# Kernel tuning notes

Measured on AMD Instinct MI355X. Metric: run time of the kernel, lower is better.

## Reference

```python
import jax, jax.numpy as jnp
import numpy as np

B, T, S, C, E, H = 4, 2048, 2048, 256, 512, 8
D = E // H
SCALE = E ** (-0.5)


def setup_inputs() -> dict:
    key = jax.random.key(0)
    ks = jax.random.split(key, 12)
    x = jax.random.normal(ks[0], (B, T, C), dtype=jnp.float32)
    context = jax.random.normal(ks[1], (B, S, E), dtype=jnp.float32)
    pad_mask = jax.random.randint(ks[2], (B, T, S), 0, 2) == 1
    p = 0.02
    # Conv1d kernel_size=1 weights stored squeezed: [out_ch, in_ch]
    w_in = jax.random.normal(ks[3], (E, C), dtype=jnp.float32) * p
    b_in = jnp.zeros((E,), dtype=jnp.float32)
    wq = jax.random.normal(ks[4], (E, E), dtype=jnp.float32) * p
    bq = jnp.zeros((E,), dtype=jnp.float32)
    wk = jax.random.normal(ks[5], (E, E), dtype=jnp.float32) * p
    bk = jnp.zeros((E,), dtype=jnp.float32)
    wv = jax.random.normal(ks[6], (E, E), dtype=jnp.float32) * p
    bv = jnp.zeros((E,), dtype=jnp.float32)
    w_out = jax.random.normal(ks[7], (C, E), dtype=jnp.float32) * p
    b_out = jnp.zeros((C,), dtype=jnp.float32)
    return {"x": x, "context": context, "pad_mask": pad_mask,
            "w_in": w_in, "b_in": b_in, "wq": wq, "bq": bq,
            "wk": wk, "bk": bk, "wv": wv, "bv": bv,
            "w_out": w_out, "b_out": b_out}


def reference(x, context, pad_mask, w_in, b_in, wq, bq, wk, bk, wv, bv, w_out, b_out):
    # proj_in: Conv1d k=1 == per-token linear on channel dim. [B,T,C] -> [B,T,E]
    xe = jnp.einsum('btc,ec->bte', x, w_in) + b_in
    Q = (xe @ wq.T + bq).reshape(B, T, H, D)       # query tokens
    K = (context @ wk.T + bk).reshape(B, S, H, D)  # key tokens
    V = (context @ wv.T + bv).reshape(B, S, H, D)
    att = jnp.einsum('bihd,bjhd->bhij', Q, K) * SCALE  # [B,H,T,S]
    att = jnp.where(pad_mask[:, None, :, :], jnp.float32(-1e9), att)
    att = jax.nn.softmax(att, axis=-1)
    out = jnp.einsum('bhij,bjhd->bihd', att, V).reshape(B, T, E)
    # proj_out: Conv1d k=1, [B,T,E] -> [B,T,C]
    out = jnp.einsum('bte,ce->btc', out, w_out) + b_out
    return out
```

## Files before the change

### kernel.cpp

```cpp
#include <hip/hip_runtime.h>
#include <cstdint>
#include <cstddef>

#define Bb 4
#define Tt 2048
#define Ssz 2048
#define Cc 256
#define Ee 512
#define Hh 8

typedef short bf8 __attribute__((ext_vector_type(8)));
typedef float f4 __attribute__((ext_vector_type(4)));

__device__ __forceinline__ unsigned short f2bf(float x) {
  unsigned int u = __float_as_uint(x);
  u += 0x7fffu + ((u >> 16) & 1u);
  return (unsigned short)(u >> 16);
}

__device__ __forceinline__ bf8 cvt8(float4 a, float4 b) {
  bf8 r;
  r[0] = (short)f2bf(a.x); r[1] = (short)f2bf(a.y);
  r[2] = (short)f2bf(a.z); r[3] = (short)f2bf(a.w);
  r[4] = (short)f2bf(b.x); r[5] = (short)f2bf(b.y);
  r[6] = (short)f2bf(b.z); r[7] = (short)f2bf(b.w);
  return r;
}

__global__ __launch_bounds__(256) void prep(const float* __restrict__ w_in,
                                            const float* __restrict__ b_in,
                                            const float* __restrict__ wq,
                                            const float* __restrict__ bq,
                                            const float* __restrict__ wk,
                                            const float* __restrict__ wv,
                                            const float* __restrict__ wo,
                                            unsigned short* __restrict__ wkvb,
                                            unsigned short* __restrict__ wob,
                                            unsigned short* __restrict__ wqin,
                                            float* __restrict__ bqinb, float qsc) {
  __shared__ unsigned short sh[128][72];
  const int bid = blockIdx.x, tid = threadIdx.x;
  if (bid < 512) {
    int i = bid * 256 + tid;
    const float* s = (i < 65536) ? wk : wv;
    int off = (i < 65536) ? i : i - 65536;
    float4 v = ((const float4*)s)[off];
    ushort4 o;
    o.x = f2bf(v.x); o.y = f2bf(v.y); o.z = f2bf(v.z); o.w = f2bf(v.w);
    ((ushort4*)wkvb)[i] = o;
  } else if (bid < 640) {
    int i = (bid - 512) * 256 + tid;
    float4 v = ((const float4*)wo)[i];
    ushort4 o;
    o.x = f2bf(v.x); o.y = f2bf(v.y); o.z = f2bf(v.z); o.w = f2bf(v.w);
    ((ushort4*)wob)[i] = o;
  } else if (bid < 672) {
    const int idx = bid - 640;
    const int m0 = (idx & 7) * 64, n0 = (idx >> 3) * 64;
    unsigned short (*As)[72] = (unsigned short (*)[72]) & sh[0][0];
    unsigned short (*Bs)[72] = (unsigned short (*)[72]) & sh[64][0];
    const int wave = tid >> 6, lane = tid & 63;
    const int lrow = lane & 15, quad = lane >> 4;
    const int wm = (wave >> 1) * 32, wn = (wave & 1) * 32;
    const int arow = tid >> 3, ac = tid & 7;
    f4 acc[2][2];
#pragma unroll
    for (int i = 0; i < 2; i++)
#pragma unroll
      for (int j = 0; j < 2; j++) {
        f4 z = {0.f, 0.f, 0.f, 0.f};
        acc[i][j] = z;
      }
    for (int kt = 0; kt < 8; kt++) {
#pragma unroll
      for (int i = 0; i < 2; i++) {
        int row = arow + i * 32;
        const float* src = wq + (size_t)(m0 + row) * Ee + kt * 64 + ac * 8;
        float4 v0 = *(const float4*)src, v1 = *(const float4*)(src + 4);
        bf8 av;
        av[0] = (short)f2bf(v0.x * qsc); av[1] = (short)f2bf(v0.y * qsc);
        av[2] = (short)f2bf(v0.z * qsc); av[3] = (short)f2bf(v0.w * qsc);
        av[4] = (short)f2bf(v1.x * qsc); av[5] = (short)f2bf(v1.y * qsc);
        av[6] = (short)f2bf(v1.z * qsc); av[7] = (short)f2bf(v1.w * qsc);
        *(bf8*)&As[row][ac * 8] = av;
        int c = n0 + row;
        bf8 bv;
#pragma unroll
        for (int k = 0; k < 8; k++)
          bv[k] = (short)f2bf(w_in[(size_t)(kt * 64 + ac * 8 + k) * Cc + c]);
        *(bf8*)&Bs[row][ac * 8] = bv;
      }
      __syncthreads();
#pragma unroll
      for (int kk = 0; kk < 2; kk++) {
        bf8 af[2], bff[2];
#pragma unroll
        for (int i = 0; i < 2; i++) af[i] = *(const bf8*)&As[wm + i * 16 + lrow][kk * 32 + quad * 8];
#pragma unroll
        for (int j = 0; j < 2; j++) bff[j] = *(const bf8*)&Bs[wn + j * 16 + lrow][kk * 32 + quad * 8];
#pragma unroll
        for (int i = 0; i < 2; i++)
#pragma unroll
          for (int j = 0; j < 2; j++)
            acc[i][j] = __builtin_amdgcn_mfma_f32_16x16x32_bf16(af[i], bff[j], acc[i][j], 0, 0, 0);
      }
      __syncthreads();
    }
#pragma unroll
    for (int j = 0; j < 2; j++)
#pragma unroll
      for (int i = 0; i < 2; i++)
#pragma unroll
        for (int r = 0; r < 4; r++)
          wqin[(size_t)(m0 + wm + i * 16 + quad * 4 + r) * Cc + n0 + wn + j * 16 + lrow] =
              f2bf(acc[i][j][r]);
  } else {
    const int o = (bid - 672) * 32 + (tid >> 3);
    const int k0 = (tid & 7) * 64;
    float s = 0.f;
#pragma unroll
    for (int i = 0; i < 16; i++) {
      float4 w = *(const float4*)(wq + (size_t)o * Ee + k0 + i * 4);
      float4 bb = *(const float4*)(b_in + k0 + i * 4);
      s += w.x * bb.x + w.y * bb.y + w.z * bb.z + w.w * bb.w;
    }
    s += __shfl_xor(s, 1);
    s += __shfl_xor(s, 2);
    s += __shfl_xor(s, 4);
    if ((tid & 7) == 0) bqinb[o] = (s + bq[o]) * qsc;
  }
}

__global__ __launch_bounds__(256) void qkv(const float* __restrict__ x,
                                           const float* __restrict__ ctx,
                                           const unsigned short* __restrict__ wqin,
                                           const float* __restrict__ bqinb,
                                           const unsigned short* __restrict__ wkv,
                                           const float* __restrict__ bk,
                                           const float* __restrict__ bv,
                                           unsigned short* __restrict__ Qb,
                                           unsigned short* __restrict__ Kb,
                                           unsigned short* __restrict__ Vt,
                                           const int* __restrict__ mask,
                                           unsigned int* __restrict__ mp) {
  __shared__ unsigned short As[128][72];
  __shared__ unsigned short Bs[128][72];
  const int bid = blockIdx.x, tid = threadIdx.x;
  if (bid >= 768) {
    int i = (bid - 768) * 256 + tid;
    const int4* src = (const int4*)mask + (size_t)i * 8;
    unsigned int w = 0;
#pragma unroll
    for (int k = 0; k < 8; k++) {
      int4 v = src[k];
      w |= (unsigned int)(v.x != 0) << (k * 4);
      w |= (unsigned int)(v.y != 0) << (k * 4 + 1);
      w |= (unsigned int)(v.z != 0) << (k * 4 + 2);
      w |= (unsigned int)(v.w != 0) << (k * 4 + 3);
    }
    mp[i] = w;
    return;
  }
  const bool isQ = bid < 256;
  const int idx = isQ ? bid : bid - 256;
  const int m0 = (idx & 63) * 128;
  const int n0 = (idx >> 6) * 128;
  const int K = isQ ? 256 : 512;
  const float* A = isQ ? x : ctx;
  const unsigned short* Bt = isQ ? wqin : wkv;

  const int wave = tid >> 6, lane = tid & 63;
  const int lrow = lane & 15, quad = lane >> 4;
  const int wm = (wave >> 1) * 64, wn = (wave & 1) * 64;
  const int arow = tid >> 3, ac = tid & 7;

  f4 acc[4][4];
#pragma unroll
  for (int i = 0; i < 4; i++)
#pragma unroll
    for (int j = 0; j < 4; j++) {
      f4 z = {0.f, 0.f, 0.f, 0.f};
      acc[i][j] = z;
    }

  float4 ap0[4], ap1[4];
  bf8 bpre[4];
#pragma unroll
  for (int i = 0; i < 4; i++) {
    const float* src = A + (size_t)(m0 + arow + i * 32) * K + ac * 8;
    ap0[i] = *(const float4*)src;
    ap1[i] = *(const float4*)(src + 4);
    bpre[i] = *(const bf8*)(Bt + (size_t)(n0 + arow + i * 32) * K + ac * 8);
  }

  const int nkt = K >> 6;
  for (int kt = 0; kt < nkt; ++kt) {
#pragma unroll
    for (int i = 0; i < 4; i++) {
      *(bf8*)&As[arow + i * 32][ac * 8] = cvt8(ap0[i], ap1[i]);
      *(bf8*)&Bs[arow + i * 32][ac * 8] = bpre[i];
    }
    __syncthreads();
    if (kt + 1 < nkt) {
      int k0 = (kt + 1) << 6;
#pragma unroll
      for (int i = 0; i < 4; i++) {
        const float* src = A + (size_t)(m0 + arow + i * 32) * K + k0 + ac * 8;
        ap0[i] = *(const float4*)src;
        ap1[i] = *(const float4*)(src + 4);
        bpre[i] = *(const bf8*)(Bt + (size_t)(n0 + arow + i * 32) * K + k0 + ac * 8);
      }
    }
#pragma unroll
    for (int kk = 0; kk < 2; kk++) {
      bf8 af[4], bff[4];
#pragma unroll
      for (int i = 0; i < 4; i++)
        af[i] = *(const bf8*)&As[wm + i * 16 + lrow][kk * 32 + quad * 8];
#pragma unroll
      for (int j = 0; j < 4; j++)
        bff[j] = *(const bf8*)&Bs[wn + j * 16 + lrow][kk * 32 + quad * 8];
#pragma unroll
      for (int i = 0; i < 4; i++)
#pragma unroll
        for (int j = 0; j < 4; j++)
          acc[i][j] = __builtin_amdgcn_mfma_f32_16x16x32_bf16(af[i], bff[j],
                                                              acc[i][j], 0, 0, 0);
    }
    __syncthreads();
  }

  if (isQ) {
#pragma unroll
    for (int j = 0; j < 4; j++) {
      int col = n0 + wn + j * 16 + lrow;
      float bvv = bqinb[col];
#pragma unroll
      for (int i = 0; i < 4; i++)
#pragma unroll
        for (int r = 0; r < 4; r++)
          Qb[(size_t)(m0 + wm + i * 16 + quad * 4 + r) * Ee + col] =
              f2bf(acc[i][j][r] + bvv);
    }
  } else if (n0 < 512) {
#pragma unroll
    for (int j = 0; j < 4; j++) {
      int col = n0 + wn + j * 16 + lrow;
      float bvv = bk[col];
#pragma unroll
      for (int i = 0; i < 4; i++)
#pragma unroll
        for (int r = 0; r < 4; r++)
          Kb[(size_t)(m0 + wm + i * 16 + quad * 4 + r) * Ee + col] =
              f2bf(acc[i][j][r] + bvv);
    }
  } else {
#pragma unroll
    for (int j = 0; j < 4; j++) {
      int d = n0 - 512 + wn + j * 16 + lrow;
      int h = d >> 6, dd = d & 63;
      float bvv = bv[d];
#pragma unroll
      for (int i = 0; i < 4; i++) {
        int tok = m0 + wm + i * 16 + quad * 4;
        int b = tok >> 11, sl = tok & 2047;
        ushort4 pk;
        pk.x = f2bf(acc[i][j][0] + bvv);
        pk.y = f2bf(acc[i][j][1] + bvv);
        pk.z = f2bf(acc[i][j][2] + bvv);
        pk.w = f2bf(acc[i][j][3] + bvv);
        *(ushort4*)(Vt + (size_t)((b * Hh + h) * 64 + dd) * Ssz + sl) = pk;
      }
    }
  }
}

template <bool OUT_BF16, int BM, int BN, int WGM>
__global__ __launch_bounds__(256) void gemm_bt(const unsigned short* __restrict__ A,
                                               const unsigned short* __restrict__ Bt,
                                               const float* __restrict__ bias0,
                                               void* __restrict__ Cout,
                                               int M, int N, int K) {
  constexpr int WGN = 4 / WGM;
  constexpr int MI = BM / (WGM * 16);
  constexpr int NJ = BN / (WGN * 16);
  constexpr int NA = BM / 32;
  constexpr int NB = BN / 32;
  __shared__ unsigned short As[BM][72];
  __shared__ unsigned short Bs[BN][72];
  const int tid = threadIdx.x;
  const int wave = tid >> 6, lane = tid & 63;
  const int lrow = lane & 15, quad = lane >> 4;
  const int wm = (wave / WGN) * (BM / WGM);
  const int wn = (wave % WGN) * (BN / WGN);
  const int m0 = blockIdx.x * BM, n0 = blockIdx.y * BN;
  const int arow = tid >> 3, ac = tid & 7;

  f4 acc[MI][NJ];
#pragma unroll
  for (int i = 0; i < MI; i++)
#pragma unroll
    for (int j = 0; j < NJ; j++) {
      f4 z = {0.f, 0.f, 0.f, 0.f};
      acc[i][j] = z;
    }

  bf8 apre[NA], bpre[NB];
#pragma unroll
  for (int i = 0; i < NA; i++)
    apre[i] = *(const bf8*)(A + (size_t)(m0 + arow + i * 32) * K + ac * 8);
#pragma unroll
  for (int i = 0; i < NB; i++)
    bpre[i] = *(const bf8*)(Bt + (size_t)(n0 + arow + i * 32) * K + ac * 8);

  const int nkt = K >> 6;
  for (int kt = 0; kt < nkt; ++kt) {
#pragma unroll
    for (int i = 0; i < NA; i++) *(bf8*)&As[arow + i * 32][ac * 8] = apre[i];
#pragma unroll
    for (int i = 0; i < NB; i++) *(bf8*)&Bs[arow + i * 32][ac * 8] = bpre[i];
    __syncthreads();
    if (kt + 1 < nkt) {
      int k0 = (kt + 1) << 6;
#pragma unroll
      for (int i = 0; i < NA; i++)
        apre[i] = *(const bf8*)(A + (size_t)(m0 + arow + i * 32) * K + k0 + ac * 8);
#pragma unroll
      for (int i = 0; i < NB; i++)
        bpre[i] = *(const bf8*)(Bt + (size_t)(n0 + arow + i * 32) * K + k0 + ac * 8);
    }
#pragma unroll
    for (int kk = 0; kk < 2; kk++) {
      bf8 af[MI], bff[NJ];
#pragma unroll
      for (int i = 0; i < MI; i++)
        af[i] = *(const bf8*)&As[wm + i * 16 + lrow][kk * 32 + quad * 8];
#pragma unroll
      for (int j = 0; j < NJ; j++)
        bff[j] = *(const bf8*)&Bs[wn + j * 16 + lrow][kk * 32 + quad * 8];
#pragma unroll
      for (int i = 0; i < MI; i++)
#pragma unroll
        for (int j = 0; j < NJ; j++)
          acc[i][j] = __builtin_amdgcn_mfma_f32_16x16x32_bf16(af[i], bff[j],
                                                              acc[i][j], 0, 0, 0);
    }
    __syncthreads();
  }

#pragma unroll
  for (int j = 0; j < NJ; j++) {
    int col = n0 + wn + j * 16 + lrow;
    float bvv = bias0 ? bias0[col] : 0.f;
#pragma unroll
    for (int i = 0; i < MI; i++) {
#pragma unroll
      for (int r = 0; r < 4; r++) {
        int row = m0 + wm + i * 16 + quad * 4 + r;
        float v = acc[i][j][r] + bvv;
        if (OUT_BF16)
          ((unsigned short*)Cout)[(size_t)row * N + col] = f2bf(v);
        else
          ((float*)Cout)[(size_t)row * N + col] = v;
      }
    }
  }
}

__global__ __launch_bounds__(256) void attn(const unsigned short* __restrict__ Q,
                                            const unsigned short* __restrict__ K,
                                            const unsigned short* __restrict__ Vt,
                                            const unsigned int* __restrict__ mp,
                                            unsigned short* __restrict__ O) {
  __shared__ unsigned short Ks[64][72];
  __shared__ unsigned short Vts[64][72];
  __shared__ unsigned short Ps[128][72];
  const int tid = threadIdx.x;
  const int wave = tid >> 6, lane = tid & 63;
  const int lrow = lane & 15, quad = lane >> 4;
  const int bid = blockIdx.x;
  const int bh = bid & 31, b = bh >> 3, h = bh & 7;
  const int t0 = (bid >> 5) * 128;
  const int arow = tid >> 3, ac = tid & 7;
  const int wm = wave * 32;

#pragma unroll
  for (int i = 0; i < 4; i++) {
    int row = arow + i * 32;
    *(bf8*)&Ps[row][ac * 8] =
        *(const bf8*)(Q + (size_t)(b * Tt + t0 + row) * Ee + h * 64 + ac * 8);
  }
  __syncthreads();
  bf8 qf[2][2];
#pragma unroll
  for (int mi = 0; mi < 2; mi++) {
    qf[mi][0] = *(const bf8*)&Ps[wm + mi * 16 + lrow][quad * 8];
    qf[mi][1] = *(const bf8*)&Ps[wm + mi * 16 + lrow][32 + quad * 8];
  }

  f4 oacc[2][4];
  f4 dacc[2];
#pragma unroll
  for (int mi = 0; mi < 2; mi++) {
    f4 z = {0.f, 0.f, 0.f, 0.f};
    dacc[mi] = z;
#pragma unroll
    for (int j = 0; j < 4; j++) oacc[mi][j] = z;
  }
  bf8 ones;
#pragma unroll
  for (int k = 0; k < 8; k++) ones[k] = (short)0x3F80;

  const unsigned short* Kbase = K + (size_t)b * Ssz * Ee + h * 64;
  const unsigned short* Vbase = Vt + (size_t)((b * Hh + h) * 64) * Ssz;
  const unsigned int* mrow0 = mp + (size_t)(b * Tt + t0 + wm + lrow) * 64;
  const unsigned int* mrow1 = mp + (size_t)(b * Tt + t0 + wm + 16 + lrow) * 64;

  bf8 kreg[2], vreg[2];
#pragma unroll
  for (int i = 0; i < 2; i++) {
    int row = arow + i * 32;
    kreg[i] = *(const bf8*)(Kbase + (size_t)row * Ee + ac * 8);
    vreg[i] = *(const bf8*)(Vbase + (size_t)row * Ssz + ac * 8);
  }

  for (int s0 = 0; s0 < Ssz; s0 += 64) {
    __syncthreads();
#pragma unroll
    for (int i = 0; i < 2; i++) {
      int row = arow + i * 32;
      *(bf8*)&Ks[row][ac * 8] = kreg[i];
      *(bf8*)&Vts[row][ac * 8] = vreg[i];
    }
    __syncthreads();
    if (s0 + 64 < Ssz) {
#pragma unroll
      for (int i = 0; i < 2; i++) {
        int row = arow + i * 32;
        kreg[i] = *(const bf8*)(Kbase + (size_t)(s0 + 64 + row) * Ee + ac * 8);
        vreg[i] = *(const bf8*)(Vbase + (size_t)row * Ssz + s0 + 64 + ac * 8);
      }
    }
    const uint2 mw0 = *(const uint2*)(mrow0 + (s0 >> 5));
    const uint2 mw1 = *(const uint2*)(mrow1 + (s0 >> 5));

#pragma unroll
    for (int sf = 0; sf < 4; sf++) {
      bf8 kf0 = *(const bf8*)&Ks[sf * 16 + lrow][quad * 8];
      bf8 kf1 = *(const bf8*)&Ks[sf * 16 + lrow][32 + quad * 8];
      f4 sa[2];
      f4 z = {0.f, 0.f, 0.f, 0.f};
      sa[0] = z; sa[1] = z;
      sa[0] = __builtin_amdgcn_mfma_f32_16x16x32_bf16(kf0, qf[0][0], sa[0], 0, 0, 0);
      sa[0] = __builtin_amdgcn_mfma_f32_16x16x32_bf16(kf1, qf[0][1], sa[0], 0, 0, 0);
      sa[1] = __builtin_amdgcn_mfma_f32_16x16x32_bf16(kf0, qf[1][0], sa[1], 0, 0, 0);
      sa[1] = __builtin_amdgcn_mfma_f32_16x16x32_bf16(kf1, qf[1][1], sa[1], 0, 0, 0);
#pragma unroll
      for (int mi = 0; mi < 2; mi++) {
        const uint2 mw = mi ? mw1 : mw0;
        const unsigned int w = (sf >= 2) ? mw.y : mw.x;
        ushort4 pk;
#pragma unroll
        for (int r = 0; r < 4; r++) {
          const unsigned int bit = (sf & 1) * 16 + quad * 4 + r;
          float e = __builtin_amdgcn_exp2f(sa[mi][r]);
          float p = ((w >> bit) & 1u) ? 0.f : e;
          unsigned short pb = (unsigned short)(__float_as_uint(p) >> 16);
          if (r == 0) pk.x = pb;
          else if (r == 1) pk.y = pb;
          else if (r == 2) pk.z = pb;
          else pk.w = pb;
        }
        *(ushort4*)&Ps[wm + mi * 16 + lrow][sf * 16 + quad * 4] = pk;
      }
    }
#pragma unroll
    for (int kk = 0; kk < 2; kk++) {
      bf8 pf[2];
#pragma unroll
      for (int mi = 0; mi < 2; mi++) {
        pf[mi] = *(const bf8*)&Ps[wm + mi * 16 + lrow][kk * 32 + quad * 8];
        dacc[mi] = __builtin_amdgcn_mfma_f32_16x16x32_bf16(pf[mi], ones, dacc[mi], 0, 0, 0);
      }
#pragma unroll
      for (int j = 0; j < 4; j++) {
        bf8 vf = *(const bf8*)&Vts[j * 16 + lrow][kk * 32 + quad * 8];
#pragma unroll
        for (int mi = 0; mi < 2; mi++)
          oacc[mi][j] = __builtin_amdgcn_mfma_f32_16x16x32_bf16(pf[mi], vf, oacc[mi][j], 0, 0, 0);
      }
    }
  }

#pragma unroll
  for (int mi = 0; mi < 2; mi++) {
#pragma unroll
    for (int r = 0; r < 4; r++) {
      float inv = 1.0f / dacc[mi][r];
      int row = b * Tt + t0 + wm + mi * 16 + quad * 4 + r;
#pragma unroll
      for (int j = 0; j < 4; j++)
        O[(size_t)row * Ee + h * 64 + j * 16 + lrow] = f2bf(oacc[mi][j][r] * inv);
    }
  }
}

extern "C" void kernel_launch(void* const* d_in, const int* in_sizes, int n_in,
                              void* d_out, int out_size, void* d_ws, size_t ws_size,
                              hipStream_t stream) {
  const float* x    = (const float*)d_in[0];
  const float* ctx  = (const float*)d_in[1];
  const int*   mask = (const int*)d_in[2];
  const float* w_in = (const float*)d_in[3];
  const float* b_in = (const float*)d_in[4];
  const float* wq   = (const float*)d_in[5];
  const float* bq   = (const float*)d_in[6];
  const float* wk   = (const float*)d_in[7];
  const float* bk   = (const float*)d_in[8];
  const float* wv   = (const float*)d_in[9];
  const float* bv   = (const float*)d_in[10];
  const float* wo   = (const float*)d_in[11];
  const float* bo   = (const float*)d_in[12];

  const float qsc = 0.04419417382415922f * 1.4426950408889634f;

  unsigned short* ws = (unsigned short*)d_ws;
  unsigned int*   maskp = (unsigned int*)ws;
  unsigned short* wkvb  = ws + 1048576;
  unsigned short* wob   = ws + 1572864;
  unsigned short* wqin  = ws + 1703936;
  float*          bqinb = (float*)(ws + 1835008);
  unsigned short* Qb    = ws + 1836032;
  unsigned short* Kb    = ws + 6030336;
  unsigned short* Vtb   = ws + 10224640;
  unsigned short* Ob    = ws + 14418944;

  prep<<<688, 256, 0, stream>>>(w_in, b_in, wq, bq, wk, wv, wo,
                                wkvb, wob, wqin, bqinb, qsc);
  qkv<<<2816, 256, 0, stream>>>(x, ctx, wqin, bqinb, wkvb, bk, bv, Qb, Kb, Vtb,
                                mask, maskp);
  attn<<<512, 256, 0, stream>>>(Qb, Kb, Vtb, maskp, Ob);
  gemm_bt<false, 64, 64, 2><<<dim3(128, 4), 256, 0, stream>>>(
      Ob, wob, bo, d_out, 8192, 256, 512);
}
```

Measured before the change: 237.5 us.

## Fuse Q projection into attention kernel, drop Q from QKV GEMM

Computes each attention block's Q tile (x times the folded W_q·W_in, per head) inside the attention kernel with MFMA before the softmax loop, instead of writing Q to global memory in the QKV kernel and reading it back. The former QKV kernel becomes a K/V-only projection plus mask packing. This removes the Q write/read round trip and 256 GEMM blocks, but adds a K=256 GEMM prologue to each of the 512 attention blocks, reusing Ps/Ks shared buffers, which may lengthen the attention kernel's critical path.

```diff
diff --git a/kernel.cpp b/kernel.cpp
--- a/kernel.cpp
+++ b/kernel.cpp
@@ -131,23 +131,19 @@
   }
 }
 
-__global__ __launch_bounds__(256) void qkv(const float* __restrict__ x,
-                                           const float* __restrict__ ctx,
-                                           const unsigned short* __restrict__ wqin,
-                                           const float* __restrict__ bqinb,
-                                           const unsigned short* __restrict__ wkv,
-                                           const float* __restrict__ bk,
-                                           const float* __restrict__ bv,
-                                           unsigned short* __restrict__ Qb,
-                                           unsigned short* __restrict__ Kb,
-                                           unsigned short* __restrict__ Vt,
-                                           const int* __restrict__ mask,
-                                           unsigned int* __restrict__ mp) {
+__global__ __launch_bounds__(256) void kv(const float* __restrict__ ctx,
+                                          const unsigned short* __restrict__ wkv,
+                                          const float* __restrict__ bk,
+                                          const float* __restrict__ bv,
+                                          unsigned short* __restrict__ Kb,
+                                          unsigned short* __restrict__ Vt,
+                                          const int* __restrict__ mask,
+                                          unsigned int* __restrict__ mp) {
   __shared__ unsigned short As[128][72];
   __shared__ unsigned short Bs[128][72];
   const int bid = blockIdx.x, tid = threadIdx.x;
-  if (bid >= 768) {
-    int i = (bid - 768) * 256 + tid;
+  if (bid >= 512) {
+    int i = (bid - 512) * 256 + tid;
     const int4* src = (const int4*)mask + (size_t)i * 8;
     unsigned int w = 0;
 #pragma unroll
@@ -161,13 +157,9 @@
     mp[i] = w;
     return;
   }
-  const bool isQ = bid < 256;
-  const int idx = isQ ? bid : bid - 256;
-  const int m0 = (idx & 63) * 128;
-  const int n0 = (idx >> 6) * 128;
-  const int K = isQ ? 256 : 512;
-  const float* A = isQ ? x : ctx;
-  const unsigned short* Bt = isQ ? wqin : wkv;
+  const int m0 = (bid & 63) * 128;
+  const int n0 = (bid >> 6) * 128;
+  const int K = 512;
 
   const int wave = tid >> 6, lane = tid & 63;
   const int lrow = lane & 15, quad = lane >> 4;
@@ -187,28 +179,27 @@
   bf8 bpre[4];
 #pragma unroll
   for (int i = 0; i < 4; i++) {
-    const float* src = A + (size_t)(m0 + arow + i * 32) * K + ac * 8;
+    const float* src = ctx + (size_t)(m0 + arow + i * 32) * K + ac * 8;
     ap0[i] = *(const float4*)src;
     ap1[i] = *(const float4*)(src + 4);
-    bpre[i] = *(const bf8*)(Bt + (size_t)(n0 + arow + i * 32) * K + ac * 8);
-  }
-
-  const int nkt = K >> 6;
-  for (int kt = 0; kt < nkt; ++kt) {
+    bpre[i] = *(const bf8*)(wkv + (size_t)(n0 + arow + i * 32) * K + ac * 8);
+  }
+
+  for (int kt = 0; kt < 8; ++kt) {
 #pragma unroll
     for (int i = 0; i < 4; i++) {
       *(bf8*)&As[arow + i * 32][ac * 8] = cvt8(ap0[i], ap1[i]);
       *(bf8*)&Bs[arow + i * 32][ac * 8] = bpre[i];
     }
     __syncthreads();
-    if (kt + 1 < nkt) {
+    if (kt + 1 < 8) {
       int k0 = (kt + 1) << 6;
 #pragma unroll
       for (int i = 0; i < 4; i++) {
-        const float* src = A + (size_t)(m0 + arow + i * 32) * K + k0 + ac * 8;
+        const float* src = ctx + (size_t)(m0 + arow + i * 32) * K + k0 + ac * 8;
         ap0[i] = *(const float4*)src;
         ap1[i] = *(const float4*)(src + 4);
-        bpre[i] = *(const bf8*)(Bt + (size_t)(n0 + arow + i * 32) * K + k0 + ac * 8);
+        bpre[i] = *(const bf8*)(wkv + (size_t)(n0 + arow + i * 32) * K + k0 + ac * 8);
       }
     }
 #pragma unroll
@@ -230,19 +221,7 @@
     __syncthreads();
   }
 
-  if (isQ) {
-#pragma unroll
-    for (int j = 0; j < 4; j++) {
-      int col = n0 + wn + j * 16 + lrow;
-      float bvv = bqinb[col];
-#pragma unroll
-      for (int i = 0; i < 4; i++)
-#pragma unroll
-        for (int r = 0; r < 4; r++)
-          Qb[(size_t)(m0 + wm + i * 16 + quad * 4 + r) * Ee + col] =
-              f2bf(acc[i][j][r] + bvv);
-    }
-  } else if (n0 < 512) {
+  if (n0 < 512) {
 #pragma unroll
     for (int j = 0; j < 4; j++) {
       int col = n0 + wn + j * 16 + lrow;
@@ -367,7 +346,9 @@
   }
 }
 
-__global__ __launch_bounds__(256) void attn(const unsigned short* __restrict__ Q,
+__global__ __launch_bounds__(256) void attn(const float* __restrict__ x,
+                                            const unsigned short* __restrict__ wqin,
+                                            const float* __restrict__ bqinb,
                                             const unsigned short* __restrict__ K,
                                             const unsigned short* __restrict__ Vt,
                                             const unsigned int* __restrict__ mp,
@@ -384,37 +365,8 @@
   const int arow = tid >> 3, ac = tid & 7;
   const int wm = wave * 32;
 
-#pragma unroll
-  for (int i = 0; i < 4; i++) {
-    int row = arow + i * 32;
-    *(bf8*)&Ps[row][ac * 8] =
-        *(const bf8*)(Q + (size_t)(b * Tt + t0 + row) * Ee + h * 64 + ac * 8);
-  }
-  __syncthreads();
-  bf8 qf[2][2];
-#pragma unroll
-  for (int mi = 0; mi < 2; mi++) {
-    qf[mi][0] = *(const bf8*)&Ps[wm + mi * 16 + lrow][quad * 8];
-    qf[mi][1] = *(const bf8*)&Ps[wm + mi * 16 + lrow][32 + quad * 8];
-  }
-
-  f4 oacc[2][4];
-  f4 dacc[2];
-#pragma unroll
-  for (int mi = 0; mi < 2; mi++) {
-    f4 z = {0.f, 0.f, 0.f, 0.f};
-    dacc[mi] = z;
-#pragma unroll
-    for (int j = 0; j < 4; j++) oacc[mi][j] = z;
-  }
-  bf8 ones;
-#pragma unroll
-  for (int k = 0; k < 8; k++) ones[k] = (short)0x3F80;
-
   const unsigned short* Kbase = K + (size_t)b * Ssz * Ee + h * 64;
   const unsigned short* Vbase = Vt + (size_t)((b * Hh + h) * 64) * Ssz;
-  const unsigned int* mrow0 = mp + (size_t)(b * Tt + t0 + wm + lrow) * 64;
-  const unsigned int* mrow1 = mp + (size_t)(b * Tt + t0 + wm + 16 + lrow) * 64;
 
   bf8 kreg[2], vreg[2];
 #pragma unroll
@@ -423,6 +375,84 @@
     kreg[i] = *(const bf8*)(Kbase + (size_t)row * Ee + ac * 8);
     vreg[i] = *(const bf8*)(Vbase + (size_t)row * Ssz + ac * 8);
   }
+
+  f4 qacc[4][2];
+#pragma unroll
+  for (int i = 0; i < 4; i++)
+#pragma unroll
+    for (int j = 0; j < 2; j++) {
+      f4 z = {0.f, 0.f, 0.f, 0.f};
+      qacc[i][j] = z;
+    }
+  for (int kt = 0; kt < 4; ++kt) {
+    if (kt) __syncthreads();
+#pragma unroll
+    for (int i = 0; i < 4; i++) {
+      const float* src = x + (size_t)(b * Tt + t0 + arow + i * 32) * Cc + kt * 64 + ac * 8;
+      float4 v0 = *(const float4*)src;
+      float4 v1 = *(const float4*)(src + 4);
+      *(bf8*)&Ps[arow + i * 32][ac * 8] = cvt8(v0, v1);
+    }
+#pragma unroll
+    for (int i = 0; i < 2; i++)
+      *(bf8*)&Ks[arow + i * 32][ac * 8] =
+          *(const bf8*)(wqin + (size_t)(h * 64 + arow + i * 32) * Cc + kt * 64 + ac * 8);
+    __syncthreads();
+#pragma unroll
+    for (int kk = 0; kk < 2; kk++) {
+      bf8 xf[2], wf[4];
+#pragma unroll
+      for (int j = 0; j < 2; j++)
+        xf[j] = *(const bf8*)&Ps[wm + j * 16 + lrow][kk * 32 + quad * 8];
+#pragma unroll
+      for (int i = 0; i < 4; i++)
+        wf[i] = *(const bf8*)&Ks[i * 16 + lrow][kk * 32 + quad * 8];
+#pragma unroll
+      for (int i = 0; i < 4; i++)
+#pragma unroll
+        for (int j = 0; j < 2; j++)
+          qacc[i][j] = __builtin_amdgcn_mfma_f32_16x16x32_bf16(wf[i], xf[j],
+                                                               qacc[i][j], 0, 0, 0);
+    }
+  }
+  __syncthreads();
+#pragma unroll
+  for (int i = 0; i < 4; i++) {
+    float4 bq4 = *(const float4*)(bqinb + h * 64 + i * 16 + quad * 4);
+#pragma unroll
+    for (int j = 0; j < 2; j++) {
+      int t = wm + j * 16 + lrow;
+      ushort4 pk;
+      pk.x = f2bf(qacc[i][j][0] + bq4.x);
+      pk.y = f2bf(qacc[i][j][1] + bq4.y);
+      pk.z = f2bf(qacc[i][j][2] + bq4.z);
+      pk.w = f2bf(qacc[i][j][3] + bq4.w);
+      *(ushort4*)&Ps[t][i * 16 + quad * 4] = pk;
+    }
+  }
+  __syncthreads();
+  bf8 qf[2][2];
+#pragma unroll
+  for (int mi = 0; mi < 2; mi++) {
+    qf[mi][0] = *(const bf8*)&Ps[wm + mi * 16 + lrow][quad * 8];
+    qf[mi][1] = *(const bf8*)&Ps[wm + mi * 16 + lrow][32 + quad * 8];
+  }
+
+  f4 oacc[2][4];
+  f4 dacc[2];
+#pragma unroll
+  for (int mi = 0; mi < 2; mi++) {
+    f4 z = {0.f, 0.f, 0.f, 0.f};
+    dacc[mi] = z;
+#pragma unroll
+    for (int j = 0; j < 4; j++) oacc[mi][j] = z;
+  }
+  bf8 ones;
+#pragma unroll
+  for (int k = 0; k < 8; k++) ones[k] = (short)0x3F80;
+
+  const unsigned int* mrow0 = mp + (size_t)(b * Tt + t0 + wm + lrow) * 64;
+  const unsigned int* mrow1 = mp + (size_t)(b * Tt + t0 + wm + 16 + lrow) * 64;
 
   for (int s0 = 0; s0 < Ssz; s0 += 64) {
     __syncthreads();
@@ -530,16 +560,14 @@
   unsigned short* wob   = ws + 1572864;
   unsigned short* wqin  = ws + 1703936;
   float*          bqinb = (float*)(ws + 1835008);
-  unsigned short* Qb    = ws + 1836032;
   unsigned short* Kb    = ws + 6030336;
   unsigned short* Vtb   = ws + 10224640;
   unsigned short* Ob    = ws + 14418944;
 
   prep<<<688, 256, 0, stream>>>(w_in, b_in, wq, bq, wk, wv, wo,
                                 wkvb, wob, wqin, bqinb, qsc);
-  qkv<<<2816, 256, 0, stream>>>(x, ctx, wqin, bqinb, wkvb, bk, bv, Qb, Kb, Vtb,
-                                mask, maskp);
-  attn<<<512, 256, 0, stream>>>(Qb, Kb, Vtb, maskp, Ob);
+  kv<<<2560, 256, 0, stream>>>(ctx, wkvb, bk, bv, Kb, Vtb, mask, maskp);
+  attn<<<512, 256, 0, stream>>>(x, wqin, bqinb, Kb, Vtb, maskp, Ob);
   gemm_bt<false, 64, 64, 2><<<dim3(128, 4), 256, 0, stream>>>(
       Ob, wob, bo, d_out, 8192, 256, 512);
 }
```

Result: slower. 244.7 us (+3.0%).

## Give each attention wave 64 query rows and pack mask bits with ballot

Applied to the files above, without the earlier changes.

The attention kernel drops to 128 threads per block, so each of its two waves now owns 64 query rows instead of 32. Every K and V fragment read from shared memory then feeds twice as many MFMAs, which is meant to cut LDS traffic per unit of compute. The cost is more accumulator registers per wave and half as many resident waves to hide latency. Separately, mask packing now has each wave read a mask row coalesced and build 64-bit words with a wave ballot, replacing the per-thread strided int4 loads and bit shifts.

```diff
diff --git a/kernel.cpp b/kernel.cpp
--- a/kernel.cpp
+++ b/kernel.cpp
@@ -147,18 +147,16 @@
   __shared__ unsigned short Bs[128][72];
   const int bid = blockIdx.x, tid = threadIdx.x;
   if (bid >= 768) {
-    int i = (bid - 768) * 256 + tid;
-    const int4* src = (const int4*)mask + (size_t)i * 8;
-    unsigned int w = 0;
-#pragma unroll
-    for (int k = 0; k < 8; k++) {
-      int4 v = src[k];
-      w |= (unsigned int)(v.x != 0) << (k * 4);
-      w |= (unsigned int)(v.y != 0) << (k * 4 + 1);
-      w |= (unsigned int)(v.z != 0) << (k * 4 + 2);
-      w |= (unsigned int)(v.w != 0) << (k * 4 + 3);
-    }
-    mp[i] = w;
+    const int lane = tid & 63;
+    const int row = (bid - 768) * 4 + (tid >> 6);
+    const int* mrow = mask + (size_t)row * Ssz;
+    unsigned long long* dst = (unsigned long long*)mp + (size_t)row * 32;
+#pragma unroll 4
+    for (int j = 0; j < 32; j++) {
+      int v = mrow[j * 64 + lane];
+      unsigned long long bal = __ballot(v != 0);
+      if (lane == 0) dst[j] = bal;
+    }
     return;
   }
   const bool isQ = bid < 256;
@@ -367,7 +365,7 @@
   }
 }
 
-__global__ __launch_bounds__(256) void attn(const unsigned short* __restrict__ Q,
+__global__ __launch_bounds__(128) void attn(const unsigned short* __restrict__ Q,
                                             const unsigned short* __restrict__ K,
                                             const unsigned short* __restrict__ Vt,
                                             const unsigned int* __restrict__ mp,
@@ -382,26 +380,26 @@
   const int bh = bid & 31, b = bh >> 3, h = bh & 7;
   const int t0 = (bid >> 5) * 128;
   const int arow = tid >> 3, ac = tid & 7;
-  const int wm = wave * 32;
-
-#pragma unroll
-  for (int i = 0; i < 4; i++) {
-    int row = arow + i * 32;
+  const int wm = wave * 64;
+
+#pragma unroll
+  for (int i = 0; i < 8; i++) {
+    int row = arow + i * 16;
     *(bf8*)&Ps[row][ac * 8] =
         *(const bf8*)(Q + (size_t)(b * Tt + t0 + row) * Ee + h * 64 + ac * 8);
   }
   __syncthreads();
-  bf8 qf[2][2];
-#pragma unroll
-  for (int mi = 0; mi < 2; mi++) {
+  bf8 qf[4][2];
+#pragma unroll
+  for (int mi = 0; mi < 4; mi++) {
     qf[mi][0] = *(const bf8*)&Ps[wm + mi * 16 + lrow][quad * 8];
     qf[mi][1] = *(const bf8*)&Ps[wm + mi * 16 + lrow][32 + quad * 8];
   }
 
-  f4 oacc[2][4];
-  f4 dacc[2];
-#pragma unroll
-  for (int mi = 0; mi < 2; mi++) {
+  f4 oacc[4][4];
+  f4 dacc[4];
+#pragma unroll
+  for (int mi = 0; mi < 4; mi++) {
     f4 z = {0.f, 0.f, 0.f, 0.f};
     dacc[mi] = z;
 #pragma unroll
@@ -413,13 +411,15 @@
 
   const unsigned short* Kbase = K + (size_t)b * Ssz * Ee + h * 64;
   const unsigned short* Vbase = Vt + (size_t)((b * Hh + h) * 64) * Ssz;
-  const unsigned int* mrow0 = mp + (size_t)(b * Tt + t0 + wm + lrow) * 64;
-  const unsigned int* mrow1 = mp + (size_t)(b * Tt + t0 + wm + 16 + lrow) * 64;
-
-  bf8 kreg[2], vreg[2];
-#pragma unroll
-  for (int i = 0; i < 2; i++) {
-    int row = arow + i * 32;
+  const unsigned int* mrow[4];
+#pragma unroll
+  for (int mi = 0; mi < 4; mi++)
+    mrow[mi] = mp + (size_t)(b * Tt + t0 + wm + mi * 16 + lrow) * 64;
+
+  bf8 kreg[4], vreg[4];
+#pragma unroll
+  for (int i = 0; i < 4; i++) {
+    int row = arow + i * 16;
     kreg[i] = *(const bf8*)(Kbase + (size_t)row * Ee + ac * 8);
     vreg[i] = *(const bf8*)(Vbase + (size_t)row * Ssz + ac * 8);
   }
@@ -427,38 +427,39 @@
   for (int s0 = 0; s0 < Ssz; s0 += 64) {
     __syncthreads();
 #pragma unroll
-    for (int i = 0; i < 2; i++) {
-      int row = arow + i * 32;
+    for (int i = 0; i < 4; i++) {
+      int row = arow + i * 16;
       *(bf8*)&Ks[row][ac * 8] = kreg[i];
       *(bf8*)&Vts[row][ac * 8] = vreg[i];
     }
     __syncthreads();
     if (s0 + 64 < Ssz) {
 #pragma unroll
-      for (int i = 0; i < 2; i++) {
-        int row = arow + i * 32;
+      for (int i = 0; i < 4; i++) {
+        int row = arow + i * 16;
         kreg[i] = *(const bf8*)(Kbase + (size_t)(s0 + 64 + row) * Ee + ac * 8);
         vreg[i] = *(const bf8*)(Vbase + (size_t)row * Ssz + s0 + 64 + ac * 8);
       }
     }
-    const uint2 mw0 = *(const uint2*)(mrow0 + (s0 >> 5));
-    const uint2 mw1 = *(const uint2*)(mrow1 + (s0 >> 5));
+    uint2 mw[4];
+#pragma unroll
+    for (int mi = 0; mi < 4; mi++) mw[mi] = *(const uint2*)(mrow[mi] + (s0 >> 5));
 
 #pragma unroll
     for (int sf = 0; sf < 4; sf++) {
       bf8 kf0 = *(const bf8*)&Ks[sf * 16 + lrow][quad * 8];
       bf8 kf1 = *(const bf8*)&Ks[sf * 16 + lrow][32 + quad * 8];
-      f4 sa[2];
-      f4 z = {0.f, 0.f, 0.f, 0.f};
-      sa[0] = z; sa[1] = z;
-      sa[0] = __builtin_amdgcn_mfma_f32_16x16x32_bf16(kf0, qf[0][0], sa[0], 0, 0, 0);
-      sa[0] = __builtin_amdgcn_mfma_f32_16x16x32_bf16(kf1, qf[0][1], sa[0], 0, 0, 0);
-      sa[1] = __builtin_amdgcn_mfma_f32_16x16x32_bf16(kf0, qf[1][0], sa[1], 0, 0, 0);
-      sa[1] = __builtin_amdgcn_mfma_f32_16x16x32_bf16(kf1, qf[1][1], sa[1], 0, 0, 0);
-#pragma unroll
-      for (int mi = 0; mi < 2; mi++) {
-        const uint2 mw = mi ? mw1 : mw0;
-        const unsigned int w = (sf >= 2) ? mw.y : mw.x;
+      f4 sa[4];
+#pragma unroll
+      for (int mi = 0; mi < 4; mi++) {
+        f4 z = {0.f, 0.f, 0.f, 0.f};
+        sa[mi] = z;
+        sa[mi] = __builtin_amdgcn_mfma_f32_16x16x32_bf16(kf0, qf[mi][0], sa[mi], 0, 0, 0);
+        sa[mi] = __builtin_amdgcn_mfma_f32_16x16x32_bf16(kf1, qf[mi][1], sa[mi], 0, 0, 0);
+      }
+#pragma unroll
+      for (int mi = 0; mi < 4; mi++) {
+        const unsigned int w = (sf >= 2) ? mw[mi].y : mw[mi].x;
         ushort4 pk;
 #pragma unroll
         for (int r = 0; r < 4; r++) {
@@ -476,9 +477,9 @@
     }
 #pragma unroll
     for (int kk = 0; kk < 2; kk++) {
-      bf8 pf[2];
-#pragma unroll
-      for (int mi = 0; mi < 2; mi++) {
+      bf8 pf[4];
+#pragma unroll
+      for (int mi = 0; mi < 4; mi++) {
         pf[mi] = *(const bf8*)&Ps[wm + mi * 16 + lrow][kk * 32 + quad * 8];
         dacc[mi] = __builtin_amdgcn_mfma_f32_16x16x32_bf16(pf[mi], ones, dacc[mi], 0, 0, 0);
       }
@@ -486,14 +487,14 @@
       for (int j = 0; j < 4; j++) {
         bf8 vf = *(const bf8*)&Vts[j * 16 + lrow][kk * 32 + quad * 8];
 #pragma unroll
-        for (int mi = 0; mi < 2; mi++)
+        for (int mi = 0; mi < 4; mi++)
           oacc[mi][j] = __builtin_amdgcn_mfma_f32_16x16x32_bf16(pf[mi], vf, oacc[mi][j], 0, 0, 0);
       }
     }
   }
 
 #pragma unroll
-  for (int mi = 0; mi < 2; mi++) {
+  for (int mi = 0; mi < 4; mi++) {
 #pragma unroll
     for (int r = 0; r < 4; r++) {
       float inv = 1.0f / dacc[mi][r];
@@ -539,7 +540,7 @@
                                 wkvb, wob, wqin, bqinb, qsc);
   qkv<<<2816, 256, 0, stream>>>(x, ctx, wqin, bqinb, wkvb, bk, bv, Qb, Kb, Vtb,
                                 mask, maskp);
-  attn<<<512, 256, 0, stream>>>(Qb, Kb, Vtb, maskp, Ob);
+  attn<<<512, 128, 0, stream>>>(Qb, Kb, Vtb, maskp, Ob);
   gemm_bt<false, 64, 64, 2><<<dim3(128, 4), 256, 0, stream>>>(
       Ob, wob, bo, d_out, 8192, 256, 512);
 }
```

After: 318.2 us. 1.34x slower.

## Fuse weight bf16 conversion into GEMM loads and prefetch attention mask words

Applied to the files above, without the earlier changes.

Drops the separate pre-conversion of wk, wv and w_out to bf16 in the prep kernel. The K/V projection and the output GEMM now read those fp32 weights directly and convert them while staging tiles into shared memory. This shrinks prep to 48 blocks and removes the workspace round trip. The Q and K/V paths in qkv become separate specialised branches. The attention kernel also prefetches the next tile's packed mask words one iteration ahead. In exchange, each GEMM block reads fp32 weights, twice the bytes, and converts them repeatedly across blocks.

```diff
diff --git a/kernel.cpp b/kernel.cpp
--- a/kernel.cpp
+++ b/kernel.cpp
@@ -31,32 +31,12 @@
                                             const float* __restrict__ b_in,
                                             const float* __restrict__ wq,
                                             const float* __restrict__ bq,
-                                            const float* __restrict__ wk,
-                                            const float* __restrict__ wv,
-                                            const float* __restrict__ wo,
-                                            unsigned short* __restrict__ wkvb,
-                                            unsigned short* __restrict__ wob,
                                             unsigned short* __restrict__ wqin,
                                             float* __restrict__ bqinb, float qsc) {
   __shared__ unsigned short sh[128][72];
   const int bid = blockIdx.x, tid = threadIdx.x;
-  if (bid < 512) {
-    int i = bid * 256 + tid;
-    const float* s = (i < 65536) ? wk : wv;
-    int off = (i < 65536) ? i : i - 65536;
-    float4 v = ((const float4*)s)[off];
-    ushort4 o;
-    o.x = f2bf(v.x); o.y = f2bf(v.y); o.z = f2bf(v.z); o.w = f2bf(v.w);
-    ((ushort4*)wkvb)[i] = o;
-  } else if (bid < 640) {
-    int i = (bid - 512) * 256 + tid;
-    float4 v = ((const float4*)wo)[i];
-    ushort4 o;
-    o.x = f2bf(v.x); o.y = f2bf(v.y); o.z = f2bf(v.z); o.w = f2bf(v.w);
-    ((ushort4*)wob)[i] = o;
-  } else if (bid < 672) {
-    const int idx = bid - 640;
-    const int m0 = (idx & 7) * 64, n0 = (idx >> 3) * 64;
+  if (bid < 32) {
+    const int m0 = (bid & 7) * 64, n0 = (bid >> 3) * 64;
     unsigned short (*As)[72] = (unsigned short (*)[72]) & sh[0][0];
     unsigned short (*Bs)[72] = (unsigned short (*)[72]) & sh[64][0];
     const int wave = tid >> 6, lane = tid & 63;
@@ -115,7 +95,7 @@
           wqin[(size_t)(m0 + wm + i * 16 + quad * 4 + r) * Cc + n0 + wn + j * 16 + lrow] =
               f2bf(acc[i][j][r]);
   } else {
-    const int o = (bid - 672) * 32 + (tid >> 3);
+    const int o = (bid - 32) * 32 + (tid >> 3);
     const int k0 = (tid & 7) * 64;
     float s = 0.f;
 #pragma unroll
@@ -135,7 +115,8 @@
                                            const float* __restrict__ ctx,
                                            const unsigned short* __restrict__ wqin,
                                            const float* __restrict__ bqinb,
-                                           const unsigned short* __restrict__ wkv,
+                                           const float* __restrict__ wk,
+                                           const float* __restrict__ wv,
                                            const float* __restrict__ bk,
                                            const float* __restrict__ bv,
                                            unsigned short* __restrict__ Qb,
@@ -161,14 +142,6 @@
     mp[i] = w;
     return;
   }
-  const bool isQ = bid < 256;
-  const int idx = isQ ? bid : bid - 256;
-  const int m0 = (idx & 63) * 128;
-  const int n0 = (idx >> 6) * 128;
-  const int K = isQ ? 256 : 512;
-  const float* A = isQ ? x : ctx;
-  const unsigned short* Bt = isQ ? wqin : wkv;
-
   const int wave = tid >> 6, lane = tid & 63;
   const int lrow = lane & 15, quad = lane >> 4;
   const int wm = (wave >> 1) * 64, wn = (wave & 1) * 64;
@@ -183,32 +156,97 @@
       acc[i][j] = z;
     }
 
-  float4 ap0[4], ap1[4];
-  bf8 bpre[4];
+  if (bid < 256) {
+    const int m0 = (bid & 63) * 128, n0 = (bid >> 6) * 128;
+    float4 ap0[4], ap1[4];
+    bf8 bpre[4];
+#pragma unroll
+    for (int i = 0; i < 4; i++) {
+      const float* src = x + (size_t)(m0 + arow + i * 32) * 256 + ac * 8;
+      ap0[i] = *(const float4*)src;
+      ap1[i] = *(const float4*)(src + 4);
+      bpre[i] = *(const bf8*)(wqin + (size_t)(n0 + arow + i * 32) * 256 + ac * 8);
+    }
+    for (int kt = 0; kt < 4; ++kt) {
+#pragma unroll
+      for (int i = 0; i < 4; i++) {
+        *(bf8*)&As[arow + i * 32][ac * 8] = cvt8(ap0[i], ap1[i]);
+        *(bf8*)&Bs[arow + i * 32][ac * 8] = bpre[i];
+      }
+      __syncthreads();
+      if (kt + 1 < 4) {
+        int k0 = (kt + 1) << 6;
+#pragma unroll
+        for (int i = 0; i < 4; i++) {
+          const float* src = x + (size_t)(m0 + arow + i * 32) * 256 + k0 + ac * 8;
+          ap0[i] = *(const float4*)src;
+          ap1[i] = *(const float4*)(src + 4);
+          bpre[i] = *(const bf8*)(wqin + (size_t)(n0 + arow + i * 32) * 256 + k0 + ac * 8);
+        }
+      }
+#pragma unroll
+      for (int kk = 0; kk < 2; kk++) {
+        bf8 af[4], bff[4];
+#pragma unroll
+        for (int i = 0; i < 4; i++)
+          af[i] = *(const bf8*)&As[wm + i * 16 + lrow][kk * 32 + quad * 8];
+#pragma unroll
+        for (int j = 0; j < 4; j++)
+          bff[j] = *(const bf8*)&Bs[wn + j * 16 + lrow][kk * 32 + quad * 8];
+#pragma unroll
+        for (int i = 0; i < 4; i++)
+#pragma unroll
+          for (int j = 0; j < 4; j++)
+            acc[i][j] = __builtin_amdgcn_mfma_f32_16x16x32_bf16(af[i], bff[j],
+                                                                acc[i][j], 0, 0, 0);
+      }
+      __syncthreads();
+    }
+#pragma unroll
+    for (int j = 0; j < 4; j++) {
+      int col = n0 + wn + j * 16 + lrow;
+      float bvv = bqinb[col];
+#pragma unroll
+      for (int i = 0; i < 4; i++)
+#pragma unroll
+        for (int r = 0; r < 4; r++)
+          Qb[(size_t)(m0 + wm + i * 16 + quad * 4 + r) * Ee + col] =
+              f2bf(acc[i][j][r] + bvv);
+    }
+    return;
+  }
+
+  const int idx = bid - 256;
+  const int m0 = (idx & 63) * 128, n0 = (idx >> 6) * 128;
+  const float* wsel = (n0 < 512) ? wk + (size_t)n0 * 512 : wv + (size_t)(n0 - 512) * 512;
+
+  float4 ap0[4], ap1[4], bp0[4], bp1[4];
 #pragma unroll
   for (int i = 0; i < 4; i++) {
-    const float* src = A + (size_t)(m0 + arow + i * 32) * K + ac * 8;
-    ap0[i] = *(const float4*)src;
-    ap1[i] = *(const float4*)(src + 4);
-    bpre[i] = *(const bf8*)(Bt + (size_t)(n0 + arow + i * 32) * K + ac * 8);
-  }
-
-  const int nkt = K >> 6;
-  for (int kt = 0; kt < nkt; ++kt) {
+    const float* srcA = ctx + (size_t)(m0 + arow + i * 32) * 512 + ac * 8;
+    ap0[i] = *(const float4*)srcA;
+    ap1[i] = *(const float4*)(srcA + 4);
+    const float* srcB = wsel + (size_t)(arow + i * 32) * 512 + ac * 8;
+    bp0[i] = *(const float4*)srcB;
+    bp1[i] = *(const float4*)(srcB + 4);
+  }
+  for (int kt = 0; kt < 8; ++kt) {
 #pragma unroll
     for (int i = 0; i < 4; i++) {
       *(bf8*)&As[arow + i * 32][ac * 8] = cvt8(ap0[i], ap1[i]);
-      *(bf8*)&Bs[arow + i * 32][ac * 8] = bpre[i];
+      *(bf8*)&Bs[arow + i * 32][ac * 8] = cvt8(bp0[i], bp1[i]);
     }
     __syncthreads();
-    if (kt + 1 < nkt) {
+    if (kt + 1 < 8) {
       int k0 = (kt + 1) << 6;
 #pragma unroll
       for (int i = 0; i < 4; i++) {
-        const float* src = A + (size_t)(m0 + arow + i * 32) * K + k0 + ac * 8;
-        ap0[i] = *(const float4*)src;
-        ap1[i] = *(const float4*)(src + 4);
-        bpre[i] = *(const bf8*)(Bt + (size_t)(n0 + arow + i * 32) * K + k0 + ac * 8);
+        const float* srcA = ctx + (size_t)(m0 + arow + i * 32) * 512 + k0 + ac * 8;
+        ap0[i] = *(const float4*)srcA;
+        ap1[i] = *(const float4*)(srcA + 4);
+        const float* srcB = wsel + (size_t)(arow + i * 32) * 512 + k0 + ac * 8;
+        bp0[i] = *(const float4*)srcB;
+        bp1[i] = *(const float4*)(srcB + 4);
       }
     }
 #pragma unroll
@@ -230,19 +268,7 @@
     __syncthreads();
   }
 
-  if (isQ) {
-#pragma unroll
-    for (int j = 0; j < 4; j++) {
-      int col = n0 + wn + j * 16 + lrow;
-      float bvv = bqinb[col];
-#pragma unroll
-      for (int i = 0; i < 4; i++)
-#pragma unroll
-        for (int r = 0; r < 4; r++)
-          Qb[(size_t)(m0 + wm + i * 16 + quad * 4 + r) * Ee + col] =
-              f2bf(acc[i][j][r] + bvv);
-    }
-  } else if (n0 < 512) {
+  if (n0 < 512) {
 #pragma unroll
     for (int j = 0; j < 4; j++) {
       int col = n0 + wn + j * 16 + lrow;
@@ -275,73 +301,68 @@
   }
 }
 
-template <bool OUT_BF16, int BM, int BN, int WGM>
-__global__ __launch_bounds__(256) void gemm_bt(const unsigned short* __restrict__ A,
-                                               const unsigned short* __restrict__ Bt,
-                                               const float* __restrict__ bias0,
-                                               void* __restrict__ Cout,
-                                               int M, int N, int K) {
-  constexpr int WGN = 4 / WGM;
-  constexpr int MI = BM / (WGM * 16);
-  constexpr int NJ = BN / (WGN * 16);
-  constexpr int NA = BM / 32;
-  constexpr int NB = BN / 32;
-  __shared__ unsigned short As[BM][72];
-  __shared__ unsigned short Bs[BN][72];
+__global__ __launch_bounds__(256) void ogemm(const unsigned short* __restrict__ A,
+                                             const float* __restrict__ wo,
+                                             const float* __restrict__ bias,
+                                             float* __restrict__ out) {
+  __shared__ unsigned short As[64][72];
+  __shared__ unsigned short Bs[64][72];
   const int tid = threadIdx.x;
   const int wave = tid >> 6, lane = tid & 63;
   const int lrow = lane & 15, quad = lane >> 4;
-  const int wm = (wave / WGN) * (BM / WGM);
-  const int wn = (wave % WGN) * (BN / WGN);
-  const int m0 = blockIdx.x * BM, n0 = blockIdx.y * BN;
+  const int wm = (wave >> 1) * 32, wn = (wave & 1) * 32;
+  const int m0 = blockIdx.x * 64, n0 = blockIdx.y * 64;
   const int arow = tid >> 3, ac = tid & 7;
 
-  f4 acc[MI][NJ];
-#pragma unroll
-  for (int i = 0; i < MI; i++)
-#pragma unroll
-    for (int j = 0; j < NJ; j++) {
+  f4 acc[2][2];
+#pragma unroll
+  for (int i = 0; i < 2; i++)
+#pragma unroll
+    for (int j = 0; j < 2; j++) {
       f4 z = {0.f, 0.f, 0.f, 0.f};
       acc[i][j] = z;
     }
 
-  bf8 apre[NA], bpre[NB];
-#pragma unroll
-  for (int i = 0; i < NA; i++)
-    apre[i] = *(const bf8*)(A + (size_t)(m0 + arow + i * 32) * K + ac * 8);
-#pragma unroll
-  for (int i = 0; i < NB; i++)
-    bpre[i] = *(const bf8*)(Bt + (size_t)(n0 + arow + i * 32) * K + ac * 8);
-
-  const int nkt = K >> 6;
-  for (int kt = 0; kt < nkt; ++kt) {
-#pragma unroll
-    for (int i = 0; i < NA; i++) *(bf8*)&As[arow + i * 32][ac * 8] = apre[i];
-#pragma unroll
-    for (int i = 0; i < NB; i++) *(bf8*)&Bs[arow + i * 32][ac * 8] = bpre[i];
+  bf8 apre[2];
+  float4 bp0[2], bp1[2];
+#pragma unroll
+  for (int i = 0; i < 2; i++) {
+    apre[i] = *(const bf8*)(A + (size_t)(m0 + arow + i * 32) * Ee + ac * 8);
+    const float* srcB = wo + (size_t)(n0 + arow + i * 32) * Ee + ac * 8;
+    bp0[i] = *(const float4*)srcB;
+    bp1[i] = *(const float4*)(srcB + 4);
+  }
+
+  for (int kt = 0; kt < 8; ++kt) {
+#pragma unroll
+    for (int i = 0; i < 2; i++) {
+      *(bf8*)&As[arow + i * 32][ac * 8] = apre[i];
+      *(bf8*)&Bs[arow + i * 32][ac * 8] = cvt8(bp0[i], bp1[i]);
+    }
     __syncthreads();
-    if (kt + 1 < nkt) {
+    if (kt + 1 < 8) {
       int k0 = (kt + 1) << 6;
 #pragma unroll
-      for (int i = 0; i < NA; i++)
-        apre[i] = *(const bf8*)(A + (size_t)(m0 + arow + i * 32) * K + k0 + ac * 8);
-#pragma unroll
-      for (int i = 0; i < NB; i++)
-        bpre[i] = *(const bf8*)(Bt + (size_t)(n0 + arow + i * 32) * K + k0 + ac * 8);
+      for (int i = 0; i < 2; i++) {
+        apre[i] = *(const bf8*)(A + (size_t)(m0 + arow + i * 32) * Ee + k0 + ac * 8);
+        const float* srcB = wo + (size_t)(n0 + arow + i * 32) * Ee + k0 + ac * 8;
+        bp0[i] = *(const float4*)srcB;
+        bp1[i] = *(const float4*)(srcB + 4);
+      }
     }
 #pragma unroll
     for (int kk = 0; kk < 2; kk++) {
-      bf8 af[MI], bff[NJ];
-#pragma unroll
-      for (int i = 0; i < MI; i++)
+      bf8 af[2], bff[2];
+#pragma unroll
+      for (int i = 0; i < 2; i++)
         af[i] = *(const bf8*)&As[wm + i * 16 + lrow][kk * 32 + quad * 8];
 #pragma unroll
-      for (int j = 0; j < NJ; j++)
+      for (int j = 0; j < 2; j++)
         bff[j] = *(const bf8*)&Bs[wn + j * 16 + lrow][kk * 32 + quad * 8];
 #pragma unroll
-      for (int i = 0; i < MI; i++)
-#pragma unroll
-        for (int j = 0; j < NJ; j++)
+      for (int i = 0; i < 2; i++)
+#pragma unroll
+        for (int j = 0; j < 2; j++)
           acc[i][j] = __builtin_amdgcn_mfma_f32_16x16x32_bf16(af[i], bff[j],
                                                               acc[i][j], 0, 0, 0);
     }
@@ -349,21 +370,15 @@
   }
 
 #pragma unroll
-  for (int j = 0; j < NJ; j++) {
+  for (int j = 0; j < 2; j++) {
     int col = n0 + wn + j * 16 + lrow;
-    float bvv = bias0 ? bias0[col] : 0.f;
-#pragma unroll
-    for (int i = 0; i < MI; i++) {
-#pragma unroll
-      for (int r = 0; r < 4; r++) {
-        int row = m0 + wm + i * 16 + quad * 4 + r;
-        float v = acc[i][j][r] + bvv;
-        if (OUT_BF16)
-          ((unsigned short*)Cout)[(size_t)row * N + col] = f2bf(v);
-        else
-          ((float*)Cout)[(size_t)row * N + col] = v;
-      }
-    }
+    float bvv = bias[col];
+#pragma unroll
+    for (int i = 0; i < 2; i++)
+#pragma unroll
+      for (int r = 0; r < 4; r++)
+        out[(size_t)(m0 + wm + i * 16 + quad * 4 + r) * Cc + col] =
+            acc[i][j][r] + bvv;
   }
 }
 
@@ -423,6 +438,9 @@
     kreg[i] = *(const bf8*)(Kbase + (size_t)row * Ee + ac * 8);
     vreg[i] = *(const bf8*)(Vbase + (size_t)row * Ssz + ac * 8);
   }
+  uint2 mw0 = *(const uint2*)(mrow0);
+  uint2 mw1 = *(const uint2*)(mrow1);
+  uint2 nmw0 = mw0, nmw1 = mw1;
 
   for (int s0 = 0; s0 < Ssz; s0 += 64) {
     __syncthreads();
@@ -440,9 +458,9 @@
         kreg[i] = *(const bf8*)(Kbase + (size_t)(s0 + 64 + row) * Ee + ac * 8);
         vreg[i] = *(const bf8*)(Vbase + (size_t)row * Ssz + s0 + 64 + ac * 8);
       }
-    }
-    const uint2 mw0 = *(const uint2*)(mrow0 + (s0 >> 5));
-    const uint2 mw1 = *(const uint2*)(mrow1 + (s0 >> 5));
+      nmw0 = *(const uint2*)(mrow0 + ((s0 + 64) >> 5));
+      nmw1 = *(const uint2*)(mrow1 + ((s0 + 64) >> 5));
+    }
 
 #pragma unroll
     for (int sf = 0; sf < 4; sf++) {
@@ -490,6 +508,8 @@
           oacc[mi][j] = __builtin_amdgcn_mfma_f32_16x16x32_bf16(pf[mi], vf, oacc[mi][j], 0, 0, 0);
       }
     }
+    mw0 = nmw0;
+    mw1 = nmw1;
   }
 
 #pragma unroll
@@ -526,20 +546,16 @@
 
   unsigned short* ws = (unsigned short*)d_ws;
   unsigned int*   maskp = (unsigned int*)ws;
-  unsigned short* wkvb  = ws + 1048576;
-  unsigned short* wob   = ws + 1572864;
-  unsigned short* wqin  = ws + 1703936;
-  float*          bqinb = (float*)(ws + 1835008);
-  unsigned short* Qb    = ws + 1836032;
-  unsigned short* Kb    = ws + 6030336;
-  unsigned short* Vtb   = ws + 10224640;
-  unsigned short* Ob    = ws + 14418944;
-
-  prep<<<688, 256, 0, stream>>>(w_in, b_in, wq, bq, wk, wv, wo,
-                                wkvb, wob, wqin, bqinb, qsc);
-  qkv<<<2816, 256, 0, stream>>>(x, ctx, wqin, bqinb, wkvb, bk, bv, Qb, Kb, Vtb,
+  unsigned short* wqin  = ws + 1048576;
+  float*          bqinb = (float*)(ws + 1179648);
+  unsigned short* Qb    = ws + 1180672;
+  unsigned short* Kb    = ws + 5374976;
+  unsigned short* Vtb   = ws + 9569280;
+  unsigned short* Ob    = ws + 13763584;
+
+  prep<<<48, 256, 0, stream>>>(w_in, b_in, wq, bq, wqin, bqinb, qsc);
+  qkv<<<2816, 256, 0, stream>>>(x, ctx, wqin, bqinb, wk, wv, bk, bv, Qb, Kb, Vtb,
                                 mask, maskp);
   attn<<<512, 256, 0, stream>>>(Qb, Kb, Vtb, maskp, Ob);
-  gemm_bt<false, 64, 64, 2><<<dim3(128, 4), 256, 0, stream>>>(
-      Ob, wob, bo, d_out, 8192, 256, 512);
-}
+  ogemm<<<dim3(128, 4), 256, 0, stream>>>(Ob, wo, bo, (float*)d_out);
+}
```

Measured after the change: 246.6 us. 3.8% more time.
